# Kernel optimization log

Hardware: AMD Instinct MI355X
Metric: run time of the kernel (lower is better)

Reference implementation:

```python
import jax, jax.numpy as jnp
import numpy as np

H, KV, HD, HID = 32, 8, 128, 4096
THETA, FACTOR, HI_FF, LO_FF, ORIG_MAX = 500000.0, 8.0, 4.0, 1.0, 8192


def _llama3_inv_freq():
    # standard Llama-3 rope scaling
    inv = 1.0 / (THETA ** (np.arange(0, HD, 2, dtype=np.float64) / HD))
    wavelen = 2.0 * np.pi / inv
    low_wl = ORIG_MAX / LO_FF
    high_wl = ORIG_MAX / HI_FF
    smooth = (ORIG_MAX / wavelen - LO_FF) / (HI_FF - LO_FF)
    scaled = np.where(wavelen > low_wl, inv / FACTOR, inv)
    mid = (wavelen <= low_wl) & (wavelen >= high_wl)
    scaled = np.where(mid, (1 - smooth) * inv / FACTOR + smooth * inv, scaled)
    return scaled.astype(np.float32)


def _rope_cos_sin(T):
    inv = _llama3_inv_freq()                       # [HD/2]
    pos = np.arange(T, dtype=np.float32)
    freqs = pos[:, None] * inv[None, :]            # [T, HD/2]
    emb = np.concatenate([freqs, freqs], axis=-1)  # [T, HD]
    return jnp.asarray(np.cos(emb)), jnp.asarray(np.sin(emb))


def _rotate_half(x):
    x1, x2 = jnp.split(x, 2, axis=-1)
    return jnp.concatenate([-x2, x1], axis=-1)


def setup_inputs() -> dict:
    key = jax.random.key(0)
    ks = jax.random.split(key, 5)
    s = 1.0 / np.sqrt(HID)
    return {
        "x": jax.random.normal(ks[0], (1, 2048, HID), jnp.float32),
        "wq": jax.random.normal(ks[1], (HID, H * HD), jnp.float32) * s,
        "wk": jax.random.normal(ks[2], (HID, KV * HD), jnp.float32) * s,
        "wv": jax.random.normal(ks[3], (HID, KV * HD), jnp.float32) * s,
        "wo": jax.random.normal(ks[4], (H * HD, HID), jnp.float32) * s,
    }


def reference(x, wq, wk, wv, wo):
    B, T, _ = x.shape
    q = (x @ wq).reshape(B, T, H, HD).transpose(0, 2, 1, 3)   # [B,H,T,D]
    k = (x @ wk).reshape(B, T, KV, HD).transpose(0, 2, 1, 3)  # [B,KV,T,D]
    v = (x @ wv).reshape(B, T, KV, HD).transpose(0, 2, 1, 3)
    cos, sin = _rope_cos_sin(T)                               # [T,D]
    q = q * cos + _rotate_half(q) * sin
    k = k * cos + _rotate_half(k) * sin
    rep = H // KV
    k = jnp.repeat(k, rep, axis=1)                            # [B,H,T,D]
    v = jnp.repeat(v, rep, axis=1)
    scores = jnp.einsum("bhtd,bhsd->bhts", q, k) * (1.0 / np.sqrt(HD))
    mask = jnp.tril(jnp.ones((T, T), dtype=bool))
    scores = jnp.where(mask, scores, -jnp.inf)
    att = jax.nn.softmax(scores, axis=-1)
    out = jnp.einsum("bhts,bhsd->bhtd", att, v)
    out = out.transpose(0, 2, 1, 3).reshape(B, T, H * HD)
    return out @ wo
```

## Files before the change

kernel.cpp:

```cpp
#include <hip/hip_runtime.h>
#include <math.h>

#define T_SEQ 2048
#define HID   4096
#define NH    32
#define NKV   8
#define HD    128
#define QCOLS (NH*HD)
#define KCOLS (NKV*HD)
#define KSTR  2048

typedef _Float16 f16;
typedef _Float16 f16x8 __attribute__((ext_vector_type(8)));
typedef _Float16 f16x4 __attribute__((ext_vector_type(4)));
typedef float f32x4 __attribute__((ext_vector_type(4)));

#define GLDS(g, l) __builtin_amdgcn_global_load_lds( \
    (const __attribute__((address_space(1))) void*)(g), \
    (__attribute__((address_space(3))) void*)(l), 16, 0, 0)

__global__ void rope_table(float* __restrict__ cosT, float* __restrict__ sinT) {
    int idx = blockIdx.x * blockDim.x + threadIdx.x;
    if (idx >= T_SEQ * 64) return;
    int t = idx >> 6, i = idx & 63;
    double inv = pow(500000.0, -(double)(2 * i) / 128.0);
    double wavelen = 6.283185307179586 / inv;
    const double lowwl = 8192.0, highwl = 2048.0;
    double scaled;
    if (wavelen > lowwl) {
        scaled = inv / 8.0;
    } else if (wavelen >= highwl) {
        double smooth = (8192.0 / wavelen - 1.0) / 3.0;
        scaled = (1.0 - smooth) * inv / 8.0 + smooth * inv;
    } else {
        scaled = inv;
    }
    float invf = (float)scaled;
    float phase = (float)t * invf;
    cosT[idx] = (float)cos((double)phase);
    sinT[idx] = (float)sin((double)phase);
}

__global__ void convert_f32_f16(const float* __restrict__ in, f16* __restrict__ out, int n8) {
    int i = blockIdx.x * blockDim.x + threadIdx.x;
    if (i >= n8) return;
    float4 a = *(const float4*)(in + (size_t)i * 8);
    float4 b = *(const float4*)(in + (size_t)i * 8 + 4);
    f16x8 v = {(f16)a.x, (f16)a.y, (f16)a.z, (f16)a.w, (f16)b.x, (f16)b.y, (f16)b.z, (f16)b.w};
    *(f16x8*)(out + (size_t)i * 8) = v;
}

__global__ __launch_bounds__(256) void transpose_f32_to_f16(const float* __restrict__ in,
                                                            f16* __restrict__ out,
                                                            int R, int ld) {
    __shared__ f16 t[64][72];
    const int tid = threadIdx.x;
    const int r0 = blockIdx.y * 64, c0 = blockIdx.x * 64;
#pragma unroll
    for (int i = 0; i < 4; ++i) {
        int r = i * 16 + (tid >> 4), c4 = (tid & 15) * 4;
        float4 v = *(const float4*)(in + (size_t)(r0 + r) * ld + c0 + c4);
        t[r][c4 + 0] = (f16)v.x; t[r][c4 + 1] = (f16)v.y;
        t[r][c4 + 2] = (f16)v.z; t[r][c4 + 3] = (f16)v.w;
    }
    __syncthreads();
    int n = tid >> 2, j0 = (tid & 3) * 16;
    f16x8 a, b;
#pragma unroll
    for (int j = 0; j < 8; ++j) { a[j] = t[j0 + j][n]; b[j] = t[j0 + 8 + j][n]; }
    *(f16x8*)(out + (size_t)(c0 + n) * R + r0 + j0) = a;
    *(f16x8*)(out + (size_t)(c0 + n) * R + r0 + j0 + 8) = b;
}

__global__ __launch_bounds__(256) void transpose_f16(const f16* __restrict__ in,
                                                     f16* __restrict__ out,
                                                     int R, int ld) {
    __shared__ f16 t[64][72];
    const int tid = threadIdx.x;
    const int r0 = blockIdx.y * 64, c0 = blockIdx.x * 64;
#pragma unroll
    for (int i = 0; i < 2; ++i) {
        int r = i * 32 + (tid >> 3), c8 = (tid & 7) * 8;
        f16x8 v = *(const f16x8*)(in + (size_t)(r0 + r) * ld + c0 + c8);
#pragma unroll
        for (int j = 0; j < 8; ++j) t[r][c8 + j] = v[j];
    }
    __syncthreads();
    int n = tid >> 2, j0 = (tid & 3) * 16;
    f16x8 a, b;
#pragma unroll
    for (int j = 0; j < 8; ++j) { a[j] = t[j0 + j][n]; b[j] = t[j0 + 8 + j][n]; }
    *(f16x8*)(out + (size_t)(c0 + n) * R + r0 + j0) = a;
    *(f16x8*)(out + (size_t)(c0 + n) * R + r0 + j0 + 8) = b;
}

template <typename OutT>
__global__ __launch_bounds__(256, 2) void gemm_f16(const f16* __restrict__ A,
                                                   const f16* __restrict__ Bt,
                                                   OutT* __restrict__ C,
                                                   int M, int ldc, int K) {
    __shared__ f16 As[128 * 32];
    __shared__ f16 Bs[128 * 32];
    const int tid = threadIdx.x;
    const int l = tid & 63;
    const int w = tid >> 6, wr = w >> 1, wc = w & 1;
    const int c16 = l & 15, g = l >> 4;
    const int m0 = blockIdx.y * 128, n0 = blockIdx.x * 128;

    f32x4 acc[4][4] = {};

    const f16* gA = A + (size_t)(m0 + (tid >> 2)) * K + (tid & 3) * 8;
    const f16* gB = Bt + (size_t)(n0 + (tid >> 2)) * K + (tid & 3) * 8;
    f16* lA = As + tid * 8;
    f16* lB = Bs + tid * 8;

    for (int k0 = 0; k0 < K; k0 += 32) {
        __syncthreads();
        GLDS(gA + k0, lA);
        GLDS(gA + (size_t)64 * K + k0, lA + 64 * 32);
        GLDS(gB + k0, lB);
        GLDS(gB + (size_t)64 * K + k0, lB + 64 * 32);
        __syncthreads();
        f16x8 af[4], bf[4];
#pragma unroll
        for (int mb = 0; mb < 4; ++mb)
            af[mb] = *(const f16x8*)(As + (wr * 64 + mb * 16 + c16) * 32 + g * 8);
#pragma unroll
        for (int nb = 0; nb < 4; ++nb)
            bf[nb] = *(const f16x8*)(Bs + (wc * 64 + nb * 16 + c16) * 32 + g * 8);
#pragma unroll
        for (int mb = 0; mb < 4; ++mb)
#pragma unroll
            for (int nb = 0; nb < 4; ++nb)
                acc[mb][nb] = __builtin_amdgcn_mfma_f32_16x16x32_f16(af[mb], bf[nb], acc[mb][nb], 0, 0, 0);
    }
#pragma unroll
    for (int mb = 0; mb < 4; ++mb)
#pragma unroll
        for (int nb = 0; nb < 4; ++nb)
#pragma unroll
            for (int r = 0; r < 4; ++r) {
                size_t row = m0 + wr * 64 + mb * 16 + g * 4 + r;
                C[row * ldc + n0 + wc * 64 + nb * 16 + c16] = (OutT)acc[mb][nb][r];
            }
}

__global__ void rope_apply_f16(f16* __restrict__ data, const float* __restrict__ cosT,
                               const float* __restrict__ sinT, int nheads, int stride) {
    int idx = blockIdx.x * blockDim.x + threadIdx.x;
    int lane = idx & 63;
    int row = idx >> 6;
    if (row >= T_SEQ * nheads) return;
    int t = row / nheads, h = row % nheads;
    f16* p = data + (size_t)t * stride + h * HD;
    float c = cosT[t * 64 + lane], s = sinT[t * 64 + lane];
    float x1 = (float)p[lane], x2 = (float)p[lane + 64];
    p[lane]      = (f16)(x1 * c - x2 * s);
    p[lane + 64] = (f16)(x2 * c + x1 * s);
}

__global__ __launch_bounds__(256, 3) void attn_f16(const f16* __restrict__ q,
                                                   const f16* __restrict__ k,
                                                   const f16* __restrict__ vt,
                                                   f16* __restrict__ outh) {
    __shared__ f16 Ks[64 * 128];
    __shared__ f16 Vs[128 * 64];
    __shared__ f16 Ps[4][16 * 72];
    const int tid = threadIdx.x;
    const int l = tid & 63, w = tid >> 6;
    const int c16 = l & 15, g = l >> 4;
    const int h = blockIdx.y, kvh = h >> 2;
    const float SCALE = 0.08838834764831845f;

    for (int pass = 0; pass < 2; ++pass) {
        const int qt = pass ? 31 - (int)blockIdx.x : (int)blockIdx.x;
        const int qrow = qt * 64 + w * 16 + c16;

        f16x8 qf[4];
        const f16* qbase = q + (size_t)qrow * QCOLS + h * HD;
#pragma unroll
        for (int ks = 0; ks < 4; ++ks) qf[ks] = *(const f16x8*)(qbase + ks * 32 + g * 8);

        f32x4 o[8] = {};
        float mrun = -INFINITY, lrun = 0.f;

        for (int ch = 0; ch <= qt; ++ch) {
            __syncthreads();
            {
                const char* kg = (const char*)(k + (size_t)(ch * 64) * KSTR + kvh * HD);
                int r = tid >> 2;
#pragma unroll
                for (int i = 0; i < 4; ++i) {
                    int b = (tid & 3) * 16 + i * 64;
                    uint4 d = *(const uint4*)(kg + (size_t)r * (KSTR * 2) + b);
                    *(uint4*)((char*)Ks + r * 256 + (b ^ ((r & 7) << 4))) = d;
                }
                const char* vg = (const char*)(vt + (size_t)(kvh * HD) * T_SEQ + ch * 64);
                int d2 = tid >> 1;
#pragma unroll
                for (int i = 0; i < 4; ++i) {
                    int b = (tid & 1) * 16 + i * 32;
                    uint4 dd = *(const uint4*)(vg + (size_t)d2 * (T_SEQ * 2) + b);
                    *(uint4*)((char*)Vs + d2 * 128 + (b ^ ((d2 & 7) << 4))) = dd;
                }
            }
            __syncthreads();

            f32x4 st[4];
            __builtin_amdgcn_s_setprio(1);
#pragma unroll
            for (int kb = 0; kb < 4; ++kb) {
                f32x4 a = {};
#pragma unroll
                for (int ks = 0; ks < 4; ++ks) {
                    int row = kb * 16 + c16;
                    f16x8 kf = *(const f16x8*)((const char*)Ks + row * 256 +
                                               ((ks * 64 + g * 16) ^ ((row & 7) << 4)));
                    a = __builtin_amdgcn_mfma_f32_16x16x32_f16(kf, qf[ks], a, 0, 0, 0);
                }
                st[kb] = a;
            }
            __builtin_amdgcn_s_setprio(0);

            float p[16];
            float cmax = -INFINITY;
            const bool diag = (ch == qt);
#pragma unroll
            for (int kb = 0; kb < 4; ++kb)
#pragma unroll
                for (int r = 0; r < 4; ++r) {
                    float s = st[kb][r] * SCALE;
                    if (diag) {
                        int key = ch * 64 + kb * 16 + g * 4 + r;
                        if (key > qrow) s = -INFINITY;
                    }
                    p[kb * 4 + r] = s;
                    cmax = fmaxf(cmax, s);
                }
            cmax = fmaxf(cmax, __shfl_xor(cmax, 16));
            cmax = fmaxf(cmax, __shfl_xor(cmax, 32));
            float mnew = fmaxf(mrun, cmax);
            float corr = __expf(mrun - mnew);
            float psum = 0.f;
#pragma unroll
            for (int i = 0; i < 16; ++i) { float e = __expf(p[i] - mnew); p[i] = e; psum += e; }
            psum += __shfl_xor(psum, 16);
            psum += __shfl_xor(psum, 32);
            lrun = lrun * corr + psum;
            mrun = mnew;
#pragma unroll
            for (int mb = 0; mb < 8; ++mb) o[mb] *= corr;

            f16* pw = Ps[w] + c16 * 72;
#pragma unroll
            for (int kb = 0; kb < 4; ++kb) {
                f16x4 q4 = {(f16)p[kb * 4], (f16)p[kb * 4 + 1], (f16)p[kb * 4 + 2], (f16)p[kb * 4 + 3]};
                *(f16x4*)(pw + kb * 16 + g * 4) = q4;
            }

            __builtin_amdgcn_s_setprio(1);
#pragma unroll
            for (int ks2 = 0; ks2 < 2; ++ks2) {
                f16x8 pf = *(const f16x8*)(Ps[w] + c16 * 72 + ks2 * 32 + g * 8);
#pragma unroll
                for (int mb = 0; mb < 8; ++mb) {
                    int row = mb * 16 + c16;
                    f16x8 vf = *(const f16x8*)((const char*)Vs + row * 128 +
                                               ((ks2 * 64 + g * 16) ^ ((row & 7) << 4)));
                    o[mb] = __builtin_amdgcn_mfma_f32_16x16x32_f16(vf, pf, o[mb], 0, 0, 0);
                }
            }
            __builtin_amdgcn_s_setprio(0);
        }

        float invl = 1.f / lrun;
        f16* ob = outh + (size_t)qrow * QCOLS + h * HD;
#pragma unroll
        for (int mb = 0; mb < 8; ++mb) {
            f16x4 v = {(f16)(o[mb][0] * invl), (f16)(o[mb][1] * invl),
                       (f16)(o[mb][2] * invl), (f16)(o[mb][3] * invl)};
            *(f16x4*)(ob + mb * 16 + g * 4) = v;
        }
    }
}

extern "C" void kernel_launch(void* const* d_in, const int* in_sizes, int n_in,
                              void* d_out, int out_size, void* d_ws, size_t ws_size,
                              hipStream_t stream) {
    const float* x  = (const float*)d_in[0];
    const float* wq = (const float*)d_in[1];
    const float* wk = (const float*)d_in[2];
    const float* wv = (const float*)d_in[3];
    const float* wo = (const float*)d_in[4];
    float* out = (float*)d_out;

    char* ws = (char*)d_ws;
    const size_t MB = 1024ULL * 1024ULL;
    float* cosT = (float*)(ws);
    float* sinT = (float*)(ws + 512 * 1024ULL);
    f16* xh   = (f16*)(ws + 1 * MB);
    f16* atth = xh;
    f16* qh   = (f16*)(ws + 17 * MB);
    f16* kvh  = (f16*)(ws + 33 * MB);
    f16* wT   = (f16*)(ws + 41 * MB);
    f16* vtb  = (f16*)(ws + 73 * MB);

    rope_table<<<dim3((T_SEQ * 64 + 255) / 256), dim3(256), 0, stream>>>(cosT, sinT);
    convert_f32_f16<<<dim3(T_SEQ * HID / 8 / 256), dim3(256), 0, stream>>>(x, xh, T_SEQ * HID / 8);

    transpose_f32_to_f16<<<dim3(QCOLS / 64, HID / 64), dim3(256), 0, stream>>>(wq, wT, HID, QCOLS);
    gemm_f16<f16><<<dim3(QCOLS / 128, T_SEQ / 128), dim3(256), 0, stream>>>(
        xh, wT, qh, T_SEQ, QCOLS, HID);

    transpose_f32_to_f16<<<dim3(KCOLS / 64, HID / 64), dim3(256), 0, stream>>>(wk, wT, HID, KCOLS);
    transpose_f32_to_f16<<<dim3(KCOLS / 64, HID / 64), dim3(256), 0, stream>>>(
        wv, wT + (size_t)KCOLS * HID, HID, KCOLS);
    gemm_f16<f16><<<dim3(KSTR / 128, T_SEQ / 128), dim3(256), 0, stream>>>(
        xh, wT, kvh, T_SEQ, KSTR, HID);

    rope_apply_f16<<<dim3(T_SEQ * NH * 64 / 256), dim3(256), 0, stream>>>(
        qh, cosT, sinT, NH, QCOLS);
    rope_apply_f16<<<dim3(T_SEQ * NKV * 64 / 256), dim3(256), 0, stream>>>(
        kvh, cosT, sinT, NKV, KSTR);

    transpose_f16<<<dim3(KCOLS / 64, T_SEQ / 64), dim3(256), 0, stream>>>(
        kvh + KCOLS, vtb, T_SEQ, KSTR);

    attn_f16<<<dim3(16, NH), dim3(256), 0, stream>>>(qh, kvh, vtb, atth);

    transpose_f32_to_f16<<<dim3(HID / 64, QCOLS / 64), dim3(256), 0, stream>>>(wo, wT, QCOLS, HID);
    gemm_f16<float><<<dim3(HID / 128, T_SEQ / 128), dim3(256), 0, stream>>>(
        atth, wT, out, T_SEQ, HID, QCOLS);
}
```

Baseline: 403.9 us.

## Double-buffer GEMM LDS tiles with K=64 stages and XOR-swizzled layout

Rewrites the f16 GEMM main loop to double-buffer A/B tiles in shared memory, issuing global-to-LDS loads for the next K slice while MFMAs run on the current one. The K step grows from 32 to 64, which halves the number of barriers. An XOR swizzle on the column offset is meant to avoid LDS bank conflicts on the fragment reads. LDS use rises to 64 KB per block, which may limit the two-blocks-per-CU launch bound and so reduce occupancy.

```diff
diff --git a/kernel.cpp b/kernel.cpp
--- a/kernel.cpp
+++ b/kernel.cpp
@@ -99,8 +99,8 @@
                                                    const f16* __restrict__ Bt,
                                                    OutT* __restrict__ C,
                                                    int M, int ldc, int K) {
-    __shared__ f16 As[128 * 32];
-    __shared__ f16 Bs[128 * 32];
+    __shared__ f16 As[2][128 * 64];
+    __shared__ f16 Bs[2][128 * 64];
     const int tid = threadIdx.x;
     const int l = tid & 63;
     const int w = tid >> 6, wr = w >> 1, wc = w & 1;
@@ -109,31 +109,53 @@
 
     f32x4 acc[4][4] = {};
 
-    const f16* gA = A + (size_t)(m0 + (tid >> 2)) * K + (tid & 3) * 8;
-    const f16* gB = Bt + (size_t)(n0 + (tid >> 2)) * K + (tid & 3) * 8;
-    f16* lA = As + tid * 8;
-    f16* lB = Bs + tid * 8;
-
-    for (int k0 = 0; k0 < K; k0 += 32) {
+    const int r_src = tid >> 3;
+    const int colswz = ((tid & 7) * 8) ^ ((r_src & 7) << 3);
+    const f16* gA = A + (size_t)(m0 + r_src) * K + colswz;
+    const f16* gB = Bt + (size_t)(n0 + r_src) * K + colswz;
+
+    auto stage = [&](f16* sA, f16* sB, int k0) {
+#pragma unroll
+        for (int i = 0; i < 4; ++i) {
+            GLDS(gA + (size_t)(i * 32) * K + k0, sA + i * 2048 + tid * 8);
+            GLDS(gB + (size_t)(i * 32) * K + k0, sB + i * 2048 + tid * 8);
+        }
+    };
+    auto compute = [&](const f16* sA, const f16* sB) {
+#pragma unroll
+        for (int kk = 0; kk < 2; ++kk) {
+            f16x8 af[4], bf[4];
+#pragma unroll
+            for (int mb = 0; mb < 4; ++mb) {
+                int row = wr * 64 + mb * 16 + c16;
+                af[mb] = *(const f16x8*)((const char*)sA + row * 128 +
+                                         ((kk * 64 + g * 16) ^ ((row & 7) << 4)));
+            }
+#pragma unroll
+            for (int nb = 0; nb < 4; ++nb) {
+                int row = wc * 64 + nb * 16 + c16;
+                bf[nb] = *(const f16x8*)((const char*)sB + row * 128 +
+                                         ((kk * 64 + g * 16) ^ ((row & 7) << 4)));
+            }
+#pragma unroll
+            for (int mb = 0; mb < 4; ++mb)
+#pragma unroll
+                for (int nb = 0; nb < 4; ++nb)
+                    acc[mb][nb] = __builtin_amdgcn_mfma_f32_16x16x32_f16(af[mb], bf[nb], acc[mb][nb], 0, 0, 0);
+        }
+    };
+
+    stage(As[0], Bs[0], 0);
+    __syncthreads();
+    int cur = 0;
+    for (int k0 = 64; k0 < K; k0 += 64) {
+        stage(As[cur ^ 1], Bs[cur ^ 1], k0);
+        compute(As[cur], Bs[cur]);
         __syncthreads();
-        GLDS(gA + k0, lA);
-        GLDS(gA + (size_t)64 * K + k0, lA + 64 * 32);
-        GLDS(gB + k0, lB);
-        GLDS(gB + (size_t)64 * K + k0, lB + 64 * 32);
-        __syncthreads();
-        f16x8 af[4], bf[4];
-#pragma unroll
-        for (int mb = 0; mb < 4; ++mb)
-            af[mb] = *(const f16x8*)(As + (wr * 64 + mb * 16 + c16) * 32 + g * 8);
-#pragma unroll
-        for (int nb = 0; nb < 4; ++nb)
-            bf[nb] = *(const f16x8*)(Bs + (wc * 64 + nb * 16 + c16) * 32 + g * 8);
-#pragma unroll
-        for (int mb = 0; mb < 4; ++mb)
-#pragma unroll
-            for (int nb = 0; nb < 4; ++nb)
-                acc[mb][nb] = __builtin_amdgcn_mfma_f32_16x16x32_f16(af[mb], bf[nb], acc[mb][nb], 0, 0, 0);
-    }
+        cur ^= 1;
+    }
+    compute(As[cur], Bs[cur]);
+
 #pragma unroll
     for (int mb = 0; mb < 4; ++mb)
 #pragma unroll
```

New measurement: 363.4 us. -10.0%, faster.
